# Optimization experiments

Measured on AMD Instinct MI355X. Metric: run time of the kernel, lower is better.

Reference implementation:

```python
import jax, jax.numpy as jnp
import numpy as np

HEADS = 16
HEAD_DIM = 64  # hidden 1024 / 16


def setup_inputs() -> dict:
    key = jax.random.key(0)
    ks = jax.random.split(key, 6)
    B, S, H = 2, 2048, 1024
    scale = 1.0 / np.sqrt(H)
    return {
        "hidden_states": jax.random.normal(ks[0], (B, S, H), jnp.float32),
        "attention_mask": jnp.zeros((B, 1, 1, S), jnp.float32),
        "Wq": jax.random.normal(ks[1], (H, H), jnp.float32) * scale,
        "bq": jax.random.normal(ks[2], (H,), jnp.float32) * 0.02,
        "Wk": jax.random.normal(ks[3], (H, H), jnp.float32) * scale,
        "Wv": jax.random.normal(ks[4], (H, H), jnp.float32) * scale,
        "bv": jax.random.normal(ks[5], (H,), jnp.float32) * 0.02,
    }


def _split_heads(x):
    # [B,S,H] -> [B,heads,S,head_dim]
    B, S, _ = x.shape
    return x.reshape(B, S, HEADS, HEAD_DIM).transpose(0, 2, 1, 3)


def reference(hidden_states, attention_mask, Wq, bq, Wk, Wv, bv):
    # Linear projections; torch nn.Linear computes x @ W.T + b. Key has NO bias.
    q = _split_heads(hidden_states @ Wq.T + bq)
    k = _split_heads(hidden_states @ Wk.T)
    v = _split_heads(hidden_states @ Wv.T + bv)
    scale = 1.0 / jnp.sqrt(jnp.asarray(HEAD_DIM, q.dtype))
    scores = jnp.einsum("bhqd,bhkd->bhqk", q * scale, k) + attention_mask
    probs = jax.nn.softmax(scores, axis=-1)  # dropout prob 0.0 -> identity
    ctx = jnp.einsum("bhqk,bhkd->bhqd", probs, v)
    B, _, S, _ = ctx.shape
    return ctx.transpose(0, 2, 1, 3).reshape(B, S, HEADS * HEAD_DIM)
```

## Files before the change

kernel.cpp:

```cpp
#include <hip/hip_runtime.h>
#include <hip/hip_bf16.h>

typedef __attribute__((ext_vector_type(4))) short bfx4;
typedef __attribute__((ext_vector_type(8))) short short8;
typedef __attribute__((ext_vector_type(4))) float floatx4;
typedef __attribute__((ext_vector_type(16))) float f32x16;
typedef __attribute__((ext_vector_type(4))) unsigned int uintx4;

constexpr int Sdim = 2048;
constexpr int Hdim = 1024;
constexpr int NH   = 16;
constexpr int HD   = 64;

__device__ __forceinline__ unsigned short f2bf(float f) {
    return (unsigned short)((__builtin_bit_cast(unsigned int, f) + 0x8000u) >> 16);
}

__device__ __forceinline__ short8 cvt8(const float* __restrict__ p) {
    uintx4 a = *(const uintx4*)p;
    uintx4 b = *(const uintx4*)(p + 4);
#pragma unroll
    for (int i = 0; i < 4; ++i) { a[i] += 0x8000u; b[i] += 0x8000u; }
    union { unsigned int u[4]; short8 s; } r;
    r.u[0] = __builtin_amdgcn_perm(a[1], a[0], 0x07060302u);
    r.u[1] = __builtin_amdgcn_perm(a[3], a[2], 0x07060302u);
    r.u[2] = __builtin_amdgcn_perm(b[1], b[0], 0x07060302u);
    r.u[3] = __builtin_amdgcn_perm(b[3], b[2], 0x07060302u);
    return r.s;
}

__device__ __forceinline__ void async16(const unsigned short* g, unsigned short* l) {
    __builtin_amdgcn_global_load_lds(
        (const __attribute__((address_space(1))) unsigned int*)g,
        (__attribute__((address_space(3))) unsigned int*)l,
        16, 0, 0);
}

__device__ __forceinline__ unsigned int cvtpk(float lo, float hi) {
    unsigned int r;
    asm("v_cvt_pk_bf16_f32 %0, %1, %2" : "=v"(r) : "v"(lo), "v"(hi));
    return r;
}

__global__ __launch_bounds__(256) void cast_kernel(
    const float* __restrict__ X,
    const float* __restrict__ Wq,
    const float* __restrict__ Wk,
    const float* __restrict__ Wv,
    unsigned short* __restrict__ xb,
    unsigned short* __restrict__ wb)
{
    constexpr int XC = (2 * Sdim * Hdim) / 8;
    constexpr int WC = (Hdim * Hdim) / 8;
    const int stride = gridDim.x * blockDim.x;
    for (int c = blockIdx.x * blockDim.x + threadIdx.x; c < XC + 3 * WC; c += stride) {
        const float* src;
        unsigned short* dst;
        if (c < XC) {
            src = X + (size_t)c * 8;
            dst = xb + (size_t)c * 8;
        } else {
            const int wc = c - XC;
            const int w  = wc / WC;
            const int o  = wc - w * WC;
            src = (w == 0 ? Wq : (w == 1 ? Wk : Wv)) + (size_t)o * 8;
            dst = wb + (size_t)w * (Hdim * Hdim) + (size_t)o * 8;
        }
        *(short8*)dst = cvt8(src);
    }
}

__global__ __launch_bounds__(256, 4) void qkv_proj_kernel(
    const unsigned short* __restrict__ wbf,
    const float* __restrict__ bq,
    const float* __restrict__ bv,
    const unsigned short* __restrict__ xbf,
    unsigned short* __restrict__ qo,
    unsigned short* __restrict__ ko,
    unsigned short* __restrict__ vo)
{
    __shared__ __align__(16) unsigned short smem[2 * 10240];

    const int tid  = threadIdx.x;
    const int wave = tid >> 6;
    const int lane = tid & 63;
    const int quad = lane >> 4;
    const int l16  = lane & 15;

    const int h  = blockIdx.x;
    const int n0 = h * 64;
    const int m0 = blockIdx.y * 64;

    floatx4 acc[3][4];
#pragma unroll
    for (int g = 0; g < 3; ++g)
#pragma unroll
        for (int mt = 0; mt < 4; ++mt) acc[g][mt] = (floatx4){0.f, 0.f, 0.f, 0.f};

    const int srow = tid >> 2;
    const int scol = (tid & 3) * 8;

    const unsigned short* Xr  = xbf + (size_t)(m0 + srow) * Hdim + scol;
    const unsigned short* Wr0 = wbf + (size_t)(n0 + srow) * Hdim + scol;
    const unsigned short* Wr1 = wbf + (size_t)(Hdim * Hdim)     + (size_t)(n0 + srow) * Hdim + scol;
    const unsigned short* Wr2 = wbf + (size_t)(2 * Hdim * Hdim) + (size_t)(n0 + srow) * Hdim + scol;

    {
        unsigned short* B0 = smem;
        *(short8*)(B0 +        srow * 40 + scol) = *(const short8*)Xr;
        *(short8*)(B0 + 2560 + srow * 40 + scol) = *(const short8*)Wr0;
        *(short8*)(B0 + 5120 + srow * 40 + scol) = *(const short8*)Wr1;
        *(short8*)(B0 + 7680 + srow * 40 + scol) = *(const short8*)Wr2;
    }

    for (int s = 0; s < 32; ++s) {
        __syncthreads();
        const unsigned short* buf = smem + (s & 1) * 10240;

        short8 px, p0, p1, p2;
        if (s < 31) {
            const int kn = (s + 1) * 32;
            px = *(const short8*)(Xr  + kn);
            p0 = *(const short8*)(Wr0 + kn);
            p1 = *(const short8*)(Wr1 + kn);
            p2 = *(const short8*)(Wr2 + kn);
        }

        const int boff = (wave * 16 + l16) * 40 + quad * 8;
        const short8 b0 = *(const short8*)(buf + 2560 + boff);
        const short8 b1 = *(const short8*)(buf + 5120 + boff);
        const short8 b2 = *(const short8*)(buf + 7680 + boff);
#pragma unroll
        for (int mt = 0; mt < 4; ++mt) {
            const short8 af = *(const short8*)(buf + (mt * 16 + l16) * 40 + quad * 8);
            acc[0][mt] = __builtin_amdgcn_mfma_f32_16x16x32_bf16(af, b0, acc[0][mt], 0, 0, 0);
            acc[1][mt] = __builtin_amdgcn_mfma_f32_16x16x32_bf16(af, b1, acc[1][mt], 0, 0, 0);
            acc[2][mt] = __builtin_amdgcn_mfma_f32_16x16x32_bf16(af, b2, acc[2][mt], 0, 0, 0);
        }

        if (s < 31) {
            unsigned short* nb = smem + ((s & 1) ^ 1) * 10240;
            *(short8*)(nb +        srow * 40 + scol) = px;
            *(short8*)(nb + 2560 + srow * 40 + scol) = p0;
            *(short8*)(nb + 5120 + srow * 40 + scol) = p1;
            *(short8*)(nb + 7680 + srow * 40 + scol) = p2;
        }
    }

    const int b  = m0 >> 11;
    const int s0 = m0 & 2047;
    const int dd = wave * 16 + l16;

    {
        const float bqv = bq[n0 + dd];
#pragma unroll
        for (int mt = 0; mt < 4; ++mt)
#pragma unroll
            for (int reg = 0; reg < 4; ++reg) {
                const int srw = s0 + mt * 16 + quad * 4 + reg;
                qo[((size_t)(b * Sdim + srw) * Hdim + n0) * 2 + dd] =
                    f2bf((acc[0][mt][reg] + bqv) * 0.125f);
            }
    }
#pragma unroll
    for (int mt = 0; mt < 4; ++mt)
#pragma unroll
        for (int reg = 0; reg < 4; ++reg) {
            const int srw = s0 + mt * 16 + quad * 4 + reg;
            ko[((size_t)(b * NH + h) * Sdim + srw) * HD + dd] = f2bf(acc[1][mt][reg]);
        }
    unsigned short* Vl = smem;
    {
        const float bvv = bv[n0 + dd];
#pragma unroll
        for (int mt = 0; mt < 4; ++mt) {
            bfx4 p;
#pragma unroll
            for (int reg = 0; reg < 4; ++reg) p[reg] = (short)f2bf(acc[2][mt][reg] + bvv);
            *(bfx4*)(Vl + dd * 74 + mt * 16 + quad * 4) = p;
        }
    }
    __syncthreads();
#pragma unroll
    for (int i = 0; i < 2; ++i) {
        const int t   = tid + 256 * i;
        const int d2  = t >> 3;
        const int off = (t & 7) * 8;
        *(short8*)(vo + ((size_t)(b * NH + h) * HD + d2) * Sdim + s0 + off) =
            *(const short8*)(Vl + d2 * 74 + off);
    }
}

__global__ __launch_bounds__(256) void attn_kernel(
    const unsigned short* __restrict__ kw,
    const unsigned short* __restrict__ vw,
    const float* __restrict__ mask,
    float* __restrict__ out)
{
    __shared__ __align__(16) unsigned short smem[16384];
    unsigned short* KtA = smem;
    unsigned short* VtA = smem + 8192;

    const int tid  = threadIdx.x;
    const int wave = tid >> 6;
    const int wq   = wave >> 1;
    const int wk   = wave & 1;
    const int lane = tid & 63;
    const int l5   = lane >> 5;
    const int q31  = lane & 31;
    const int m7l  = lane & 7;

    const int flat = blockIdx.x;
    const int bh   = flat & 31;
    const int b    = bh >> 4;
    const int h    = bh & 15;
    const int q0   = (flat >> 5) * 64;

    const unsigned short* K  = kw + (size_t)bh * Sdim * HD;
    const unsigned short* Vg = vw + (size_t)bh * HD * Sdim;
    const float* mg = mask + (size_t)b * Sdim;

    constexpr float SHIFT = 12.0f;

    short8 qf[4];
    {
        const unsigned short* qsrc = (const unsigned short*)out;
        const size_t qbase =
            ((size_t)(b * Sdim + q0 + wq * 32 + q31) * Hdim + h * HD) * 2;
#pragma unroll
        for (int i = 0; i < 4; ++i)
            qf[i] = *(const short8*)(qsrc + qbase + i * 16 + l5 * 8);
    }

    const int rk = wave * 16 + (lane >> 3);
    const int sw = ((lane & 7) ^ (rk & 7)) * 8;
    const unsigned short* kgp = K  + (size_t)rk * HD   + sw;
    const unsigned short* vgp = Vg + (size_t)rk * Sdim + sw;

    {
        unsigned short* Kb = KtA + wave * 1024;
        unsigned short* Vb = VtA + wave * 1024;
        async16(kgp,            Kb);
        async16(kgp + 8 * HD,   Kb + 512);
        async16(vgp,            Vb);
        async16(vgp + 8 * Sdim, Vb + 512);
        kgp += (size_t)64 * HD;
        vgp += 64;
    }

    int kOff[4], vOff[4];
#pragma unroll
    for (int i = 0; i < 4; ++i)
        kOff[i] = (wk * 32 + q31) * 64 + (((2 * i + l5) ^ m7l) * 8);
#pragma unroll
    for (int dblk = 0; dblk < 2; ++dblk)
#pragma unroll
        for (int kc = 0; kc < 2; ++kc)
            vOff[dblk * 2 + kc] =
                (dblk * 32 + q31) * 64 + (((wk * 4 + 2 * kc + l5) ^ m7l) * 8);

    const float* mgp = mg + wk * 32 + l5 * 4;

    float lsum = 0.f;
    f32x16 oT[2];
#pragma unroll
    for (int dblk = 0; dblk < 2; ++dblk)
#pragma unroll
        for (int r = 0; r < 16; ++r) oT[dblk][r] = 0.f;

    for (int it = 0; it < 32; ++it) {
        __syncthreads();
        const int kt = it * 64;
        const unsigned short* Kb = KtA + (it & 1) * 4096;
        const unsigned short* Vb = VtA + (it & 1) * 4096;

        if (it < 31) {
            unsigned short* Kn = KtA + ((it & 1) ^ 1) * 4096 + wave * 1024;
            unsigned short* Vn = VtA + ((it & 1) ^ 1) * 4096 + wave * 1024;
            async16(kgp,            Kn);
            async16(kgp + 8 * HD,   Kn + 512);
            async16(vgp,            Vn);
            async16(vgp + 8 * Sdim, Vn + 512);
            kgp += (size_t)64 * HD;
            vgp += 64;
        }

        f32x16 st;
#pragma unroll
        for (int r = 0; r < 16; ++r) st[r] = 0.f;
#pragma unroll
        for (int i = 0; i < 4; ++i) {
            const short8 ka = *(const short8*)(Kb + kOff[i]);
            st = __builtin_amdgcn_mfma_f32_32x32x16_bf16(ka, qf[i], st, 0, 0, 0);
        }

        unsigned int w[8];
#pragma unroll
        for (int j = 0; j < 4; ++j) {
            const floatx4 mv = *(const floatx4*)(mgp + kt + j * 8);
            float e[4];
#pragma unroll
            for (int r = 0; r < 4; ++r) {
                e[r] = __expf(st[j * 4 + r] + (mv[r] - SHIFT));
                lsum += e[r];
            }
            w[2 * j]     = cvtpk(e[0], e[1]);
            w[2 * j + 1] = cvtpk(e[2], e[3]);
        }

        union { unsigned int u[4]; short8 s; } pb0, pb1;
        {
            const unsigned int p0 = __shfl_xor(w[0], 32);
            const unsigned int p1 = __shfl_xor(w[1], 32);
            const unsigned int p2 = __shfl_xor(w[2], 32);
            const unsigned int p3 = __shfl_xor(w[3], 32);
            pb0.u[0] = l5 ? p2 : w[0];
            pb0.u[1] = l5 ? p3 : w[1];
            pb0.u[2] = l5 ? w[2] : p0;
            pb0.u[3] = l5 ? w[3] : p1;
        }
        {
            const unsigned int p4 = __shfl_xor(w[4], 32);
            const unsigned int p5 = __shfl_xor(w[5], 32);
            const unsigned int p6 = __shfl_xor(w[6], 32);
            const unsigned int p7 = __shfl_xor(w[7], 32);
            pb1.u[0] = l5 ? p6 : w[4];
            pb1.u[1] = l5 ? p7 : w[5];
            pb1.u[2] = l5 ? w[6] : p4;
            pb1.u[3] = l5 ? w[7] : p5;
        }

#pragma unroll
        for (int dblk = 0; dblk < 2; ++dblk) {
            const short8 va0 = *(const short8*)(Vb + vOff[dblk * 2 + 0]);
            oT[dblk] = __builtin_amdgcn_mfma_f32_32x32x16_bf16(va0, pb0.s, oT[dblk], 0, 0, 0);
            const short8 va1 = *(const short8*)(Vb + vOff[dblk * 2 + 1]);
            oT[dblk] = __builtin_amdgcn_mfma_f32_32x32x16_bf16(va1, pb1.s, oT[dblk], 0, 0, 0);
        }
    }

    lsum += __shfl_xor(lsum, 32);

    __syncthreads();

    float* Ored = (float*)smem;
    float* Lred = Ored + 64 * 68;
    const int qrow = wq * 32 + q31;
    if (wk == 0) {
#pragma unroll
        for (int dblk = 0; dblk < 2; ++dblk)
#pragma unroll
            for (int j = 0; j < 4; ++j) {
                floatx4 v;
#pragma unroll
                for (int r = 0; r < 4; ++r) v[r] = oT[dblk][j * 4 + r];
                *(floatx4*)(Ored + (size_t)qrow * 68 + dblk * 32 + j * 8 + l5 * 4) = v;
            }
        if (lane < 32) Lred[qrow] = lsum;
    }
    __syncthreads();
    if (wk == 1) {
        const float linv = 1.0f / (lsum + Lred[qrow]);
#pragma unroll
        for (int dblk = 0; dblk < 2; ++dblk)
#pragma unroll
            for (int j = 0; j < 4; ++j) {
                const floatx4 o =
                    *(const floatx4*)(Ored + (size_t)qrow * 68 + dblk * 32 + j * 8 + l5 * 4);
                floatx4 r;
#pragma unroll
                for (int t = 0; t < 4; ++t)
                    r[t] = (o[t] + oT[dblk][j * 4 + t]) * linv;
                *(floatx4*)(out + (size_t)(b * Sdim + q0 + qrow) * Hdim
                            + h * HD + dblk * 32 + j * 8 + l5 * 4) = r;
            }
    }
}

extern "C" void kernel_launch(void* const* d_in, const int* in_sizes, int n_in,
                              void* d_out, int out_size, void* d_ws, size_t ws_size,
                              hipStream_t stream) {
    const float* X    = (const float*)d_in[0];
    const float* mask = (const float*)d_in[1];
    const float* Wq   = (const float*)d_in[2];
    const float* bq   = (const float*)d_in[3];
    const float* Wk   = (const float*)d_in[4];
    const float* Wv   = (const float*)d_in[5];
    const float* bv   = (const float*)d_in[6];
    float* out = (float*)d_out;

    unsigned short* kws = (unsigned short*)d_ws;
    unsigned short* vws = kws + (size_t)4096 * 1024;
    unsigned short* xb  = vws + (size_t)4096 * 1024;
    unsigned short* wb  = xb  + (size_t)2 * Sdim * Hdim;

    cast_kernel<<<dim3(2048), 256, 0, stream>>>(X, Wq, Wk, Wv, xb, wb);
    qkv_proj_kernel<<<dim3(16, 64), 256, 0, stream>>>(
        wb, bq, bv, xb, (unsigned short*)d_out, kws, vws);
    attn_kernel<<<dim3(1024), 256, 0, stream>>>(
        kws, vws, mask, out);
}
```

Before: 191.7 us.

## Use async global-to-LDS loads with XOR swizzle and permlane32 swaps

```diff
diff --git a/kernel.cpp b/kernel.cpp
--- a/kernel.cpp
+++ b/kernel.cpp
@@ -79,7 +79,7 @@
     unsigned short* __restrict__ ko,
     unsigned short* __restrict__ vo)
 {
-    __shared__ __align__(16) unsigned short smem[2 * 10240];
+    __shared__ __align__(16) unsigned short smem[2 * 8192];
 
     const int tid  = threadIdx.x;
     const int wave = tid >> 6;
@@ -97,53 +97,47 @@
 #pragma unroll
         for (int mt = 0; mt < 4; ++mt) acc[g][mt] = (floatx4){0.f, 0.f, 0.f, 0.f};
 
-    const int srow = tid >> 2;
-    const int scol = (tid & 3) * 8;
-
-    const unsigned short* Xr  = xbf + (size_t)(m0 + srow) * Hdim + scol;
-    const unsigned short* Wr0 = wbf + (size_t)(n0 + srow) * Hdim + scol;
-    const unsigned short* Wr1 = wbf + (size_t)(Hdim * Hdim)     + (size_t)(n0 + srow) * Hdim + scol;
-    const unsigned short* Wr2 = wbf + (size_t)(2 * Hdim * Hdim) + (size_t)(n0 + srow) * Hdim + scol;
-
-    {
-        unsigned short* B0 = smem;
-        *(short8*)(B0 +        srow * 40 + scol) = *(const short8*)Xr;
-        *(short8*)(B0 + 2560 + srow * 40 + scol) = *(const short8*)Wr0;
-        *(short8*)(B0 + 5120 + srow * 40 + scol) = *(const short8*)Wr1;
-        *(short8*)(B0 + 7680 + srow * 40 + scol) = *(const short8*)Wr2;
-    }
+    const int drow   = lane >> 2;
+    const int dchunk = lane & 3;
+    const int fD     = (drow >> 1) & 3;
+    const unsigned short* gbase = (wave == 0)
+        ? xbf + (size_t)m0 * Hdim
+        : wbf + (size_t)(wave - 1) * (Hdim * Hdim) + (size_t)n0 * Hdim;
+    const unsigned short* gp =
+        gbase + (size_t)drow * Hdim + ((dchunk ^ fD) * 8);
+
+    {
+        unsigned short* db = smem + wave * 2048;
+#pragma unroll
+        for (int j = 0; j < 4; ++j)
+            async16(gp + (size_t)(j * 16) * Hdim, db + j * 512);
+    }
+
+    const int fR   = (l16 >> 1) & 3;
+    const int cswz = (quad ^ fR) * 8;
+    const int boff = (wave * 16 + l16) * 32 + cswz;
 
     for (int s = 0; s < 32; ++s) {
         __syncthreads();
-        const unsigned short* buf = smem + (s & 1) * 10240;
-
-        short8 px, p0, p1, p2;
+        const unsigned short* buf = smem + (s & 1) * 8192;
+
         if (s < 31) {
-            const int kn = (s + 1) * 32;
-            px = *(const short8*)(Xr  + kn);
-            p0 = *(const short8*)(Wr0 + kn);
-            p1 = *(const short8*)(Wr1 + kn);
-            p2 = *(const short8*)(Wr2 + kn);
-        }
-
-        const int boff = (wave * 16 + l16) * 40 + quad * 8;
-        const short8 b0 = *(const short8*)(buf + 2560 + boff);
-        const short8 b1 = *(const short8*)(buf + 5120 + boff);
-        const short8 b2 = *(const short8*)(buf + 7680 + boff);
+            unsigned short* nb = smem + ((s & 1) ^ 1) * 8192 + wave * 2048;
+            const unsigned short* g = gp + (s + 1) * 32;
+#pragma unroll
+            for (int j = 0; j < 4; ++j)
+                async16(g + (size_t)(j * 16) * Hdim, nb + j * 512);
+        }
+
+        const short8 b0 = *(const short8*)(buf + 2048 + boff);
+        const short8 b1 = *(const short8*)(buf + 4096 + boff);
+        const short8 b2 = *(const short8*)(buf + 6144 + boff);
 #pragma unroll
         for (int mt = 0; mt < 4; ++mt) {
-            const short8 af = *(const short8*)(buf + (mt * 16 + l16) * 40 + quad * 8);
+            const short8 af = *(const short8*)(buf + (mt * 16 + l16) * 32 + cswz);
             acc[0][mt] = __builtin_amdgcn_mfma_f32_16x16x32_bf16(af, b0, acc[0][mt], 0, 0, 0);
             acc[1][mt] = __builtin_amdgcn_mfma_f32_16x16x32_bf16(af, b1, acc[1][mt], 0, 0, 0);
             acc[2][mt] = __builtin_amdgcn_mfma_f32_16x16x32_bf16(af, b2, acc[2][mt], 0, 0, 0);
-        }
-
-        if (s < 31) {
-            unsigned short* nb = smem + ((s & 1) ^ 1) * 10240;
-            *(short8*)(nb +        srow * 40 + scol) = px;
-            *(short8*)(nb + 2560 + srow * 40 + scol) = p0;
-            *(short8*)(nb + 5120 + srow * 40 + scol) = p1;
-            *(short8*)(nb + 7680 + srow * 40 + scol) = p2;
         }
     }
 
@@ -308,27 +302,13 @@
             w[2 * j + 1] = cvtpk(e[2], e[3]);
         }
 
+        asm("v_permlane32_swap_b32 %0, %1" : "+v"(w[0]), "+v"(w[2]));
+        asm("v_permlane32_swap_b32 %0, %1" : "+v"(w[1]), "+v"(w[3]));
+        asm("v_permlane32_swap_b32 %0, %1" : "+v"(w[4]), "+v"(w[6]));
+        asm("v_permlane32_swap_b32 %0, %1" : "+v"(w[5]), "+v"(w[7]));
         union { unsigned int u[4]; short8 s; } pb0, pb1;
-        {
-            const unsigned int p0 = __shfl_xor(w[0], 32);
-            const unsigned int p1 = __shfl_xor(w[1], 32);
-            const unsigned int p2 = __shfl_xor(w[2], 32);
-            const unsigned int p3 = __shfl_xor(w[3], 32);
-            pb0.u[0] = l5 ? p2 : w[0];
-            pb0.u[1] = l5 ? p3 : w[1];
-            pb0.u[2] = l5 ? w[2] : p0;
-            pb0.u[3] = l5 ? w[3] : p1;
-        }
-        {
-            const unsigned int p4 = __shfl_xor(w[4], 32);
-            const unsigned int p5 = __shfl_xor(w[5], 32);
-            const unsigned int p6 = __shfl_xor(w[6], 32);
-            const unsigned int p7 = __shfl_xor(w[7], 32);
-            pb1.u[0] = l5 ? p6 : w[4];
-            pb1.u[1] = l5 ? p7 : w[5];
-            pb1.u[2] = l5 ? w[6] : p4;
-            pb1.u[3] = l5 ? w[7] : p5;
-        }
+#pragma unroll
+        for (int r = 0; r < 4; ++r) { pb0.u[r] = w[r]; pb1.u[r] = w[4 + r]; }
 
 #pragma unroll
         for (int dblk = 0; dblk < 2; ++dblk) {
```

Result: no change. 189.5 us (-1.1%).
